# Optimization experiments

Measured on AMD Instinct MI355X. Metric: run time of the kernel, lower is better.

## Reference

```python
import jax, jax.numpy as jnp
import numpy as np

D_MODEL = 1024
D_COND = 512
N_HEADS = 16
D_HEAD = D_MODEL // N_HEADS
DIM_FF = 4 * D_MODEL
EPS = 1e-5


def setup_inputs() -> dict:
    key = jax.random.key(0)
    ks = jax.random.split(key, 12)
    B, S = 2, 2048
    s = 0.02
    return {
        "x": jax.random.normal(ks[0], (B, S, D_MODEL), jnp.float32),
        "cond": jax.random.normal(ks[1], (B, S, D_COND), jnp.float32),
        # AdaLN1 proj (stored as (in, out) so y = h @ W + b)
        "p1_w": jax.random.normal(ks[2], (D_COND, 2 * D_MODEL), jnp.float32) * s,
        "p1_b": jax.random.normal(ks[3], (2 * D_MODEL,), jnp.float32) * s,
        "qkv_w": jax.random.normal(ks[4], (D_MODEL, 3 * D_MODEL), jnp.float32) * s,
        "attn_out_w": jax.random.normal(ks[5], (D_MODEL, D_MODEL), jnp.float32) * s,
        "p2_w": jax.random.normal(ks[6], (D_COND, 2 * D_MODEL), jnp.float32) * s,
        "p2_b": jax.random.normal(ks[7], (2 * D_MODEL,), jnp.float32) * s,
        "ffn_w1": jax.random.normal(ks[8], (D_MODEL, DIM_FF), jnp.float32) * s,
        "ffn_b1": jax.random.normal(ks[9], (DIM_FF,), jnp.float32) * s,
        "ffn_w2": jax.random.normal(ks[10], (DIM_FF, D_MODEL), jnp.float32) * s,
        "ffn_b2": jax.random.normal(ks[11], (D_MODEL,), jnp.float32) * s,
    }


def _adaln(x, cond, w, b):
    # LayerNorm without affine, then (1+gamma)*xn + beta with gamma,beta from cond
    gb = jax.nn.silu(cond) @ w + b            # (B,S,2D)
    gamma, beta = jnp.split(gb, 2, axis=-1)
    mu = jnp.mean(x, axis=-1, keepdims=True)
    var = jnp.mean((x - mu) ** 2, axis=-1, keepdims=True)
    xn = (x - mu) * jax.lax.rsqrt(var + EPS)
    return xn * (1.0 + gamma) + beta


def reference(x, cond, p1_w, p1_b, qkv_w, attn_out_w, p2_w, p2_b,
              ffn_w1, ffn_b1, ffn_w2, ffn_b2):
    B, S, D = x.shape
    H, d = N_HEADS, D_HEAD
    scale = d ** -0.5

    residual = x
    h = _adaln(x, cond, p1_w, p1_b)
    qkv = h @ qkv_w                            # (B,S,3D)
    q, k, v = jnp.split(qkv, 3, axis=-1)
    q = q.reshape(B, S, H, d).transpose(0, 2, 1, 3)   # (B,H,S,d)
    k = k.reshape(B, S, H, d).transpose(0, 2, 1, 3)
    v = v.reshape(B, S, H, d).transpose(0, 2, 1, 3)

    scores = jnp.einsum("bhqd,bhkd->bhqk", q, k) * scale
    attn = jax.nn.softmax(scores, axis=-1)
    out = jnp.einsum("bhqk,bhkd->bhqd", attn, v)      # (B,H,S,d)
    out = out.transpose(0, 2, 1, 3).reshape(B, S, D)
    x = residual + out @ attn_out_w

    residual = x
    h = _adaln(x, cond, p2_w, p2_b)
    ff = jax.nn.gelu(h @ ffn_w1 + ffn_b1, approximate=False) @ ffn_w2 + ffn_b2
    return residual + ff
```

## Files before the change

### kernel.cpp

```cpp
#include <hip/hip_runtime.h>
#include <math.h>

#define D_MODEL 1024
#define SEQ 2048
#define NTOK 4096

typedef __attribute__((ext_vector_type(8))) short bf16x8;
typedef __attribute__((ext_vector_type(4))) float f32x4;

__device__ __forceinline__ unsigned short f2bf(float f) {
    union { float f; unsigned u; } v; v.f = f;
    unsigned r = v.u + 0x7FFFu + ((v.u >> 16) & 1u);
    return (unsigned short)(r >> 16);
}
__device__ __forceinline__ float bf2f(unsigned short u) {
    union { unsigned u; float f; } v; v.u = ((unsigned)u) << 16; return v.f;
}
__device__ __forceinline__ unsigned cvt_pk_bf16(float x, float y) {
    unsigned r;
    asm("v_cvt_pk_bf16_f32 %0, %1, %2" : "=v"(r) : "v"(x), "v"(y));
    return r;
}

__device__ __forceinline__ void ld_g2l(const void* g, void* l) {
    __builtin_amdgcn_global_load_lds(
        (const __attribute__((address_space(1))) void*)g,
        (__attribute__((address_space(3))) void*)l, 16, 0, 0);
}

__global__ __launch_bounds__(256) void prep_weights(
    const float* __restrict__ p1, const float* __restrict__ p2,
    const float* __restrict__ qkvw, const float* __restrict__ attnw,
    const float* __restrict__ f1, const float* __restrict__ f2,
    const float* __restrict__ cond,
    unsigned short* __restrict__ wt_cond, unsigned short* __restrict__ wt_qkv,
    unsigned short* __restrict__ wt_attn, unsigned short* __restrict__ wt_ffn1,
    unsigned short* __restrict__ wt_ffn2, unsigned short* __restrict__ siluc)
{
    const int t = blockIdx.x;
    if (t >= 3584) {
        const int base = (t - 3584) * 1024 + threadIdx.x;
#pragma unroll
        for (int i = 0; i < 4; i++) {
            const int idx = base + i * 256;
            float4 v = ((const float4*)cond)[idx];
            ushort4 o;
            o.x = f2bf(v.x / (1.f + expf(-v.x)));
            o.y = f2bf(v.y / (1.f + expf(-v.y)));
            o.z = f2bf(v.z / (1.f + expf(-v.z)));
            o.w = f2bf(v.w / (1.f + expf(-v.w)));
            ((ushort4*)siluc)[idx] = o;
        }
        return;
    }
    const float* src; unsigned short* dst; int K, N, lt;
    if (t < 512)       { src = (t < 256) ? p1 : p2;
                         dst = wt_cond + (t < 256 ? 0 : 2048 * 512);
                         K = 512;  N = 2048; lt = t & 255; }
    else if (t < 1280) { src = qkvw;  dst = wt_qkv;  K = 1024; N = 3072; lt = t - 512; }
    else if (t < 1536) { src = attnw; dst = wt_attn; K = 1024; N = 1024; lt = t - 1280; }
    else if (t < 2560) { src = f1;    dst = wt_ffn1; K = 1024; N = 4096; lt = t - 1536; }
    else               { src = f2;    dst = wt_ffn2; K = 4096; N = 1024; lt = t - 2560; }
    const int ntile = N >> 6;
    const int n0 = (lt % ntile) * 64, k0 = (lt / ntile) * 64;

    __shared__ float tile[64][65];
    const int tx = threadIdx.x & 15, ty = threadIdx.x >> 4;
#pragma unroll
    for (int i = 0; i < 4; i++) {
        const int k = ty + i * 16;
        float4 v = *(const float4*)&src[(size_t)(k0 + k) * N + n0 + tx * 4];
        tile[k][tx * 4 + 0] = v.x; tile[k][tx * 4 + 1] = v.y;
        tile[k][tx * 4 + 2] = v.z; tile[k][tx * 4 + 3] = v.w;
    }
    __syncthreads();
#pragma unroll
    for (int i = 0; i < 4; i++) {
        const int n = ty + i * 16;
        ushort4 o;
        o.x = f2bf(tile[tx * 4 + 0][n]); o.y = f2bf(tile[tx * 4 + 1][n]);
        o.z = f2bf(tile[tx * 4 + 2][n]); o.w = f2bf(tile[tx * 4 + 3][n]);
        *(ushort4*)&dst[(size_t)(n0 + n) * K + k0 + tx * 4] = o;
    }
}

#define EPI_GB   0
#define EPI_QKV  1
#define EPI_PROJ 2
#define EPI_FFN1 3
#define EPI_FFN2 4
#define EPI_PART 5

template<int EPI, int BM, int SPLIT = 1>
__global__ __launch_bounds__(256, 4) void gemm_bf16(
    const unsigned short* __restrict__ A,
    const unsigned short* __restrict__ Bt,
    const float* __restrict__ bias, const float* __restrict__ bias2,
    const float* __restrict__ res,
    void* __restrict__ Cv,
    unsigned short* __restrict__ qb, unsigned short* __restrict__ kb,
    unsigned short* __restrict__ vtb,
    int K)
{
    constexpr int WM = BM / 2;
    constexpr int MT = WM / 16;
    __shared__ __align__(16) unsigned short As[BM * 64];
    __shared__ __align__(16) unsigned short Bs[128 * 64];
    const int tid = threadIdx.x;
    const int lane = tid & 63, w = tid >> 6;
    const int cc = lane & 15, quad = lane >> 4;
    const int wm = (w >> 1) * WM, wn = (w & 1) * 64;
    const int m0 = blockIdx.y * BM, n0 = blockIdx.x * 128;
    const int kslice = K / SPLIT;
    const int kbeg = (SPLIT > 1) ? (int)blockIdx.z * kslice : 0;

    f32x4 acc[MT][4];
#pragma unroll
    for (int i = 0; i < MT; i++)
#pragma unroll
        for (int j = 0; j < 4; j++) acc[i][j] = (f32x4)0.f;

    for (int k0 = kbeg; k0 < kbeg + kslice; k0 += 64) {
        __syncthreads();
#pragma unroll
        for (int i = 0; i < BM / 32; i++) {
            const int idx = i * 256 + tid;
            const int row = idx >> 3, c = idx & 7;
            const int kc = (c ^ (row & 7)) << 3;
            ld_g2l(&A[(size_t)(m0 + row) * K + k0 + kc], &As[idx << 3]);
        }
#pragma unroll
        for (int i = 0; i < 4; i++) {
            const int idx = i * 256 + tid;
            const int row = idx >> 3, c = idx & 7;
            const int kc = (c ^ (row & 7)) << 3;
            ld_g2l(&Bt[(size_t)(n0 + row) * K + k0 + kc], &Bs[idx << 3]);
        }
        __syncthreads();
#pragma unroll
        for (int ks = 0; ks < 2; ks++) {
            bf16x8 af[MT], bfr[4];
            const int pc = (((ks << 2) | quad) ^ (cc & 7)) << 3;
#pragma unroll
            for (int t = 0; t < MT; t++)
                af[t]  = *(const bf16x8*)&As[(wm + t * 16 + cc) * 64 + pc];
#pragma unroll
            for (int t = 0; t < 4; t++)
                bfr[t] = *(const bf16x8*)&Bs[(wn + t * 16 + cc) * 64 + pc];
#pragma unroll
            for (int mt = 0; mt < MT; mt++)
#pragma unroll
                for (int nt = 0; nt < 4; nt++)
                    acc[mt][nt] = __builtin_amdgcn_mfma_f32_16x16x32_bf16(
                        af[mt], bfr[nt], acc[mt][nt], 0, 0, 0);
        }
    }

    if (EPI == EPI_GB) {
        unsigned short* C = (unsigned short*)Cv;
#pragma unroll
        for (int mt = 0; mt < MT; mt++)
#pragma unroll
        for (int r = 0; r < 4; r++) {
            const int m = m0 + wm + mt * 16 + quad * 4 + r;
#pragma unroll
            for (int nt = 0; nt < 4; nt++) {
                const int n = n0 + wn + nt * 16 + cc;
                const float b = (n < 2048) ? bias[n] : bias2[n - 2048];
                C[(size_t)m * 4096 + n] = f2bf(acc[mt][nt][r] + b);
            }
        }
    } else if (EPI == EPI_PROJ) {
        float* C = (float*)Cv;
#pragma unroll
        for (int mt = 0; mt < MT; mt++)
#pragma unroll
        for (int r = 0; r < 4; r++) {
            const int m = m0 + wm + mt * 16 + quad * 4 + r;
#pragma unroll
            for (int nt = 0; nt < 4; nt++) {
                const int n = n0 + wn + nt * 16 + cc;
                C[(size_t)m * 1024 + n] = acc[mt][nt][r] + res[(size_t)m * 1024 + n];
            }
        }
    } else if (EPI == EPI_FFN1) {
        unsigned short* C = (unsigned short*)Cv;
#pragma unroll
        for (int mt = 0; mt < MT; mt++)
#pragma unroll
        for (int r = 0; r < 4; r++) {
            const int m = m0 + wm + mt * 16 + quad * 4 + r;
#pragma unroll
            for (int nt = 0; nt < 4; nt++) {
                const int n = n0 + wn + nt * 16 + cc;
                float v = acc[mt][nt][r] + bias[n];
                const float u = v + 0.044715f * v * v * v;
                const float g = v / (1.f + exp2f(-2.3022084f * u));
                C[(size_t)m * 4096 + n] = f2bf(g);
            }
        }
    } else if (EPI == EPI_PART) {
        unsigned short* C = (unsigned short*)Cv + (size_t)blockIdx.z * (4096ull * 1024ull);
#pragma unroll
        for (int mt = 0; mt < MT; mt++)
#pragma unroll
        for (int r = 0; r < 4; r++) {
            const int m = m0 + wm + mt * 16 + quad * 4 + r;
#pragma unroll
            for (int nt = 0; nt < 4; nt++) {
                const int n = n0 + wn + nt * 16 + cc;
                C[(size_t)m * 1024 + n] = f2bf(acc[mt][nt][r]);
            }
        }
    } else if (EPI == EPI_FFN2) {
        float* C = (float*)Cv;
#pragma unroll
        for (int mt = 0; mt < MT; mt++)
#pragma unroll
        for (int r = 0; r < 4; r++) {
            const int m = m0 + wm + mt * 16 + quad * 4 + r;
#pragma unroll
            for (int nt = 0; nt < 4; nt++) {
                const int n = n0 + wn + nt * 16 + cc;
                C[(size_t)m * 1024 + n] = acc[mt][nt][r] + bias[n] + res[(size_t)m * 1024 + n];
            }
        }
    } else {
        const int region = n0 >> 10;
        const int b = m0 >> 11;
        if (region < 2) {
            unsigned short* dst = region ? kb : qb;
            const float sc = region ? 1.0f : 0.125f * 1.44269504088896340736f;
#pragma unroll
            for (int mt = 0; mt < MT; mt++)
#pragma unroll
            for (int r = 0; r < 4; r++) {
                const int m = m0 + wm + mt * 16 + quad * 4 + r;
                const int s = m & 2047;
#pragma unroll
                for (int nt = 0; nt < 4; nt++) {
                    const int n = (n0 + wn + nt * 16 + cc) & 1023;
                    const int hh = n >> 6, d = n & 63;
                    dst[(((size_t)b * 16 + hh) * 2048 + s) * 64 + d] =
                        f2bf(acc[mt][nt][r] * sc);
                }
            }
        } else {
            const int sb = (m0 + wm) & 2047;
#pragma unroll
            for (int mt = 0; mt < MT; mt++) {
                const int kpos = sb + ((mt >> 1) << 5) + (quad << 3) + ((mt & 1) << 2);
#pragma unroll
                for (int nt = 0; nt < 4; nt++) {
                    const int n = (n0 + wn + nt * 16 + cc) & 1023;
                    const int hh = n >> 6, d = n & 63;
                    ushort4 o;
                    o.x = f2bf(acc[mt][nt][0]); o.y = f2bf(acc[mt][nt][1]);
                    o.z = f2bf(acc[mt][nt][2]); o.w = f2bf(acc[mt][nt][3]);
                    *(ushort4*)&vtb[(((size_t)b * 16 + hh) * 64 + d) * 2048 + kpos] = o;
                }
            }
        }
    }
}

__global__ __launch_bounds__(256) void merge_ffn2(
    const unsigned short* __restrict__ P, const float* __restrict__ x1,
    const float* __restrict__ b2, float* __restrict__ out)
{
    const size_t idx = (size_t)blockIdx.x * 1024 + (size_t)threadIdx.x * 4;
    const int n = (int)(idx & 1023);
    float4 xv = *(const float4*)&x1[idx];
    float4 bv = *(const float4*)&b2[n];
    float s0 = 0.f, s1 = 0.f, s2 = 0.f, s3 = 0.f;
#pragma unroll
    for (int z = 0; z < 4; z++) {
        ushort4 p = *(const ushort4*)&P[z * (4096ull * 1024ull) + idx];
        s0 += bf2f(p.x); s1 += bf2f(p.y); s2 += bf2f(p.z); s3 += bf2f(p.w);
    }
    float4 o;
    o.x = xv.x + bv.x + s0;
    o.y = xv.y + bv.y + s1;
    o.z = xv.z + bv.z + s2;
    o.w = xv.w + bv.w + s3;
    *(float4*)&out[idx] = o;
}

__global__ __launch_bounds__(512) void attn_mfma(
    const unsigned short* __restrict__ qb, const unsigned short* __restrict__ kb,
    const unsigned short* __restrict__ vtb,
    unsigned short* __restrict__ Op0, unsigned short* __restrict__ Op1,
    unsigned short* __restrict__ Op2, unsigned short* __restrict__ Op3,
    float* __restrict__ lp)
{
    __shared__ __align__(16) unsigned short ks[64 * 64];
    __shared__ __align__(16) unsigned short vts[64 * 64];

    const int tid = threadIdx.x;
    const int lane = tid & 63, w = tid >> 6;
    const int c = lane & 15, quad = lane >> 4;
    const int bh = blockIdx.y;
    const int q0 = blockIdx.x * 256;
    const int z = blockIdx.z;
    const int kk0 = z * 512;

    bf16x8 qf[2][2];
#pragma unroll
    for (int qs = 0; qs < 2; qs++) {
        const size_t base = (((size_t)bh * 2048) + q0 + w * 32 + qs * 16 + c) * 64 + quad * 8;
        qf[qs][0] = *(const bf16x8*)&qb[base];
        qf[qs][1] = *(const bf16x8*)&qb[base + 32];
    }

    bf16x8 ones;
#pragma unroll
    for (int i = 0; i < 8; i++) ones[i] = (short)0x3F80;

    f32x4 of[2][4];
#pragma unroll
    for (int qs = 0; qs < 2; qs++)
#pragma unroll
        for (int i = 0; i < 4; i++) of[qs][i] = (f32x4)0.f;
    f32x4 lf[2];
    lf[0] = (f32x4)0.f; lf[1] = (f32x4)0.f;

    const size_t kbase = ((size_t)bh * 2048) * 64;
    const size_t vbase = ((size_t)bh * 64) * 2048;

    const int srow = tid >> 3, spc = tid & 7;
    const int slc = spc ^ (srow & 7);

    for (int kk = kk0; kk < kk0 + 512; kk += 64) {
        __syncthreads();
        ld_g2l(&kb[kbase + (size_t)(kk + srow) * 64 + slc * 8], &ks[tid << 3]);
        ld_g2l(&vtb[vbase + (size_t)srow * 2048 + kk + slc * 8], &vts[tid << 3]);
        __syncthreads();

        f32x4 sc[2][4];
#pragma unroll
        for (int qs = 0; qs < 2; qs++)
#pragma unroll
            for (int t = 0; t < 4; t++) sc[qs][t] = (f32x4)0.f;
#pragma unroll
        for (int t = 0; t < 4; t++) {
#pragma unroll
            for (int kh = 0; kh < 2; kh++) {
                const int phys = ((kh * 4 + quad) ^ (c & 7)) << 3;
                bf16x8 kf = *(const bf16x8*)&ks[(t * 16 + c) * 64 + phys];
#pragma unroll
                for (int qs = 0; qs < 2; qs++)
                    sc[qs][t] = __builtin_amdgcn_mfma_f32_16x16x32_bf16(
                        kf, qf[qs][kh], sc[qs][t], 0, 0, 0);
            }
        }

        bf16x8 pb[2][2];
#pragma unroll
        for (int qs = 0; qs < 2; qs++) {
#pragma unroll
            for (int t = 0; t < 4; t++)
#pragma unroll
                for (int r = 0; r < 4; r++)
                    sc[qs][t][r] = exp2f(sc[qs][t][r]);
#pragma unroll
            for (int kh = 0; kh < 2; kh++) {
                union { int4 i; bf16x8 v; } u;
                u.i.x = cvt_pk_bf16(sc[qs][2 * kh][0],     sc[qs][2 * kh][1]);
                u.i.y = cvt_pk_bf16(sc[qs][2 * kh][2],     sc[qs][2 * kh][3]);
                u.i.z = cvt_pk_bf16(sc[qs][2 * kh + 1][0], sc[qs][2 * kh + 1][1]);
                u.i.w = cvt_pk_bf16(sc[qs][2 * kh + 1][2], sc[qs][2 * kh + 1][3]);
                pb[qs][kh] = u.v;
            }
        }

#pragma unroll
        for (int qs = 0; qs < 2; qs++)
#pragma unroll
            for (int kh = 0; kh < 2; kh++)
                lf[qs] = __builtin_amdgcn_mfma_f32_16x16x32_bf16(
                    ones, pb[qs][kh], lf[qs], 0, 0, 0);

#pragma unroll
        for (int dt = 0; dt < 4; dt++) {
#pragma unroll
            for (int kh = 0; kh < 2; kh++) {
                const int phys = ((kh * 4 + quad) ^ (c & 7)) << 3;
                bf16x8 vf = *(const bf16x8*)&vts[(dt * 16 + c) * 64 + phys];
#pragma unroll
                for (int qs = 0; qs < 2; qs++)
                    of[qs][dt] = __builtin_amdgcn_mfma_f32_16x16x32_bf16(
                        vf, pb[qs][kh], of[qs][dt], 0, 0, 0);
            }
        }
    }

    unsigned short* Op = (z == 0) ? Op0 : (z == 1) ? Op1 : (z == 2) ? Op2 : Op3;
    const int b = bh >> 4, hh = bh & 15;
#pragma unroll
    for (int qs = 0; qs < 2; qs++) {
        const int q = q0 + w * 32 + qs * 16 + c;
        if (lane < 16)
            lp[((size_t)z * 32 + bh) * 2048 + q] = lf[qs][0];
        const size_t row = (size_t)(b * 2048 + q);
#pragma unroll
        for (int dt = 0; dt < 4; dt++) {
            ushort4 o;
            o.x = f2bf(of[qs][dt][0]); o.y = f2bf(of[qs][dt][1]);
            o.z = f2bf(of[qs][dt][2]); o.w = f2bf(of[qs][dt][3]);
            *(ushort4*)&Op[row * 1024 + hh * 64 + dt * 16 + quad * 4] = o;
        }
    }
}

__global__ __launch_bounds__(256) void merge_attn(
    const unsigned short* __restrict__ Op0, const unsigned short* __restrict__ Op1,
    const unsigned short* __restrict__ Op2, const unsigned short* __restrict__ Op3,
    const float* __restrict__ lp, unsigned short* __restrict__ attnb)
{
    const int row = blockIdx.x;
    const int b = row >> 11, s = row & 2047;
    const int tid = threadIdx.x;
    const int n = tid * 4, h = tid >> 4;
    float lsum = 0.f;
#pragma unroll
    for (int z = 0; z < 4; z++)
        lsum += lp[((size_t)z * 32 + b * 16 + h) * 2048 + s];
    const float inv = 1.f / lsum;
    const size_t off = (size_t)row * 1024 + n;
    ushort4 a0 = *(const ushort4*)&Op0[off];
    ushort4 a1 = *(const ushort4*)&Op1[off];
    ushort4 a2 = *(const ushort4*)&Op2[off];
    ushort4 a3 = *(const ushort4*)&Op3[off];
    ushort4 o;
    o.x = f2bf((bf2f(a0.x) + bf2f(a1.x) + bf2f(a2.x) + bf2f(a3.x)) * inv);
    o.y = f2bf((bf2f(a0.y) + bf2f(a1.y) + bf2f(a2.y) + bf2f(a3.y)) * inv);
    o.z = f2bf((bf2f(a0.z) + bf2f(a1.z) + bf2f(a2.z) + bf2f(a3.z)) * inv);
    o.w = f2bf((bf2f(a0.w) + bf2f(a1.w) + bf2f(a2.w) + bf2f(a3.w)) * inv);
    *(ushort4*)&attnb[off] = o;
}

__global__ __launch_bounds__(256) void adaln_bf(
    const float* __restrict__ x, const unsigned short* __restrict__ gb, int gboff,
    unsigned short* __restrict__ h)
{
    const int row = blockIdx.x;
    const float* xr = x + (size_t)row * D_MODEL;
    float4 v = ((const float4*)xr)[threadIdx.x];
    float s = v.x + v.y + v.z + v.w;
    float ss = v.x * v.x + v.y * v.y + v.z * v.z + v.w * v.w;
#pragma unroll
    for (int off = 1; off < 64; off <<= 1) {
        s  += __shfl_xor(s, off, 64);
        ss += __shfl_xor(ss, off, 64);
    }
    __shared__ float red[8];
    const int wave = threadIdx.x >> 6;
    if ((threadIdx.x & 63) == 0) { red[wave] = s; red[4 + wave] = ss; }
    __syncthreads();
    s  = red[0] + red[1] + red[2] + red[3];
    ss = red[4] + red[5] + red[6] + red[7];
    const float mu = s * (1.f / 1024.f);
    const float var = ss * (1.f / 1024.f) - mu * mu;
    const float rstd = rsqrtf(var + 1e-5f);
    const int c = threadIdx.x * 4;
    ushort4 g4 = *(const ushort4*)&gb[(size_t)row * 4096 + gboff + c];
    ushort4 b4 = *(const ushort4*)&gb[(size_t)row * 4096 + gboff + 1024 + c];
    ushort4 o;
    o.x = f2bf((v.x - mu) * rstd * (1.f + bf2f(g4.x)) + bf2f(b4.x));
    o.y = f2bf((v.y - mu) * rstd * (1.f + bf2f(g4.y)) + bf2f(b4.y));
    o.z = f2bf((v.z - mu) * rstd * (1.f + bf2f(g4.z)) + bf2f(b4.z));
    o.w = f2bf((v.w - mu) * rstd * (1.f + bf2f(g4.w)) + bf2f(b4.w));
    *(ushort4*)&h[(size_t)row * 1024 + c] = o;
}

extern "C" void kernel_launch(void* const* d_in, const int* in_sizes, int n_in,
                              void* d_out, int out_size, void* d_ws, size_t ws_size,
                              hipStream_t stream)
{
    const float* x      = (const float*)d_in[0];
    const float* cond   = (const float*)d_in[1];
    const float* p1_w   = (const float*)d_in[2];
    const float* p1_b   = (const float*)d_in[3];
    const float* qkv_w  = (const float*)d_in[4];
    const float* attn_w = (const float*)d_in[5];
    const float* p2_w   = (const float*)d_in[6];
    const float* p2_b   = (const float*)d_in[7];
    const float* ffn_w1 = (const float*)d_in[8];
    const float* ffn_b1 = (const float*)d_in[9];
    const float* ffn_w2 = (const float*)d_in[10];
    const float* ffn_b2 = (const float*)d_in[11];
    float* out = (float*)d_out;

    char* ws = (char*)d_ws;
    const size_t MB = 1024ull * 1024ull;
    unsigned short* wt_cond = (unsigned short*)(ws);
    unsigned short* wt_qkv  = (unsigned short*)(ws + 4 * MB);
    unsigned short* wt_attn = (unsigned short*)(ws + 10 * MB);
    unsigned short* wt_ffn1 = (unsigned short*)(ws + 12 * MB);
    unsigned short* wt_ffn2 = (unsigned short*)(ws + 20 * MB);
    unsigned short* siluc   = (unsigned short*)(ws + 28 * MB);
    unsigned short* gb      = (unsigned short*)(ws + 32 * MB);
    unsigned short* h       = (unsigned short*)(ws + 64 * MB);
    float*          x1      = (float*)(ws + 72 * MB);
    unsigned short* qb      = (unsigned short*)(ws + 88 * MB);
    unsigned short* kb      = (unsigned short*)(ws + 96 * MB);
    unsigned short* vtb     = (unsigned short*)(ws + 104 * MB);
    unsigned short* attnb   = (unsigned short*)(ws + 112 * MB);
    unsigned short* ff1     = (unsigned short*)(ws + 88 * MB);
    unsigned short* Op0     = (unsigned short*)(ws);
    unsigned short* Op1     = (unsigned short*)(ws + 64 * MB);
    unsigned short* Op2     = (unsigned short*)(ws + 72 * MB);
    unsigned short* Op3     = (unsigned short*)(ws + 80 * MB);
    float*          lp      = (float*)(ws + 28 * MB);
    unsigned short* Pff     = (unsigned short*)(ws + 32 * MB);

    dim3 blk(256);

    prep_weights<<<dim3(4096), blk, 0, stream>>>(
        p1_w, p2_w, qkv_w, attn_w, ffn_w1, ffn_w2, cond,
        wt_cond, wt_qkv, wt_attn, wt_ffn1, wt_ffn2, siluc);

    gemm_bf16<EPI_GB, 128><<<dim3(32, 32), blk, 0, stream>>>(
        siluc, wt_cond, p1_b, p2_b, nullptr, gb, nullptr, nullptr, nullptr, 512);
    adaln_bf<<<NTOK, blk, 0, stream>>>(x, gb, 0, h);
    gemm_bf16<EPI_QKV, 128><<<dim3(24, 32), blk, 0, stream>>>(
        h, wt_qkv, nullptr, nullptr, nullptr, nullptr, qb, kb, vtb, 1024);
    attn_mfma<<<dim3(SEQ / 256, 32, 4), dim3(512), 0, stream>>>(
        qb, kb, vtb, Op0, Op1, Op2, Op3, lp);
    merge_attn<<<dim3(NTOK), blk, 0, stream>>>(Op0, Op1, Op2, Op3, lp, attnb);
    gemm_bf16<EPI_PROJ, 64><<<dim3(8, 64), blk, 0, stream>>>(
        attnb, wt_attn, nullptr, nullptr, x, x1, nullptr, nullptr, nullptr, 1024);
    adaln_bf<<<NTOK, blk, 0, stream>>>(x1, gb, 2048, h);
    gemm_bf16<EPI_FFN1, 128><<<dim3(32, 32), blk, 0, stream>>>(
        h, wt_ffn1, ffn_b1, nullptr, nullptr, ff1, nullptr, nullptr, nullptr, 1024);
    gemm_bf16<EPI_PART, 64, 4><<<dim3(8, 64, 4), blk, 0, stream>>>(
        ff1, wt_ffn2, nullptr, nullptr, nullptr, Pff, nullptr, nullptr, nullptr, 4096);
    merge_ffn2<<<dim3(4096), blk, 0, stream>>>(Pff, x1, ffn_b2, out);
}
```

Measured before the change: 399.4 us.

## Double-buffer LDS in GEMMs, reduce FFN2 split-K, and prioritize MFMA in attention

Adds an optional double-buffered LDS path to the bf16 GEMM so the next K-tile's loads are issued while the current tile is computed, with one barrier per iteration. This path is enabled for the attention output projection and FFN2. FFN2 now uses BM=128 and split-K 2 instead of BM=64 and split-K 4, and the merge kernel reads two partial buffers instead of four. The attention kernel drops the explicit zeroing of score accumulators by feeding a zero operand directly, and raises wave priority around its MFMA sections. Double buffering doubles LDS use per block, which may reduce occupancy. With a single barrier, the async global-to-LDS loads may also need extra waitcnt handling to stay correct.

```diff
diff --git a/kernel.cpp b/kernel.cpp
--- a/kernel.cpp
+++ b/kernel.cpp
@@ -91,7 +91,7 @@
 #define EPI_FFN2 4
 #define EPI_PART 5
 
-template<int EPI, int BM, int SPLIT = 1>
+template<int EPI, int BM, bool DBUF = false, int SPLIT = 1>
 __global__ __launch_bounds__(256, 4) void gemm_bf16(
     const unsigned short* __restrict__ A,
     const unsigned short* __restrict__ Bt,
@@ -104,8 +104,9 @@
 {
     constexpr int WM = BM / 2;
     constexpr int MT = WM / 16;
-    __shared__ __align__(16) unsigned short As[BM * 64];
-    __shared__ __align__(16) unsigned short Bs[128 * 64];
+    constexpr int NB = DBUF ? 2 : 1;
+    __shared__ __align__(16) unsigned short As[NB][BM * 64];
+    __shared__ __align__(16) unsigned short Bs[NB][128 * 64];
     const int tid = threadIdx.x;
     const int lane = tid & 63, w = tid >> 6;
     const int cc = lane & 15, quad = lane >> 4;
@@ -120,39 +121,57 @@
 #pragma unroll
         for (int j = 0; j < 4; j++) acc[i][j] = (f32x4)0.f;
 
-    for (int k0 = kbeg; k0 < kbeg + kslice; k0 += 64) {
-        __syncthreads();
+    auto stage = [&](int buf, int k0) {
 #pragma unroll
         for (int i = 0; i < BM / 32; i++) {
             const int idx = i * 256 + tid;
             const int row = idx >> 3, c = idx & 7;
             const int kc = (c ^ (row & 7)) << 3;
-            ld_g2l(&A[(size_t)(m0 + row) * K + k0 + kc], &As[idx << 3]);
+            ld_g2l(&A[(size_t)(m0 + row) * K + k0 + kc], &As[buf][idx << 3]);
         }
 #pragma unroll
         for (int i = 0; i < 4; i++) {
             const int idx = i * 256 + tid;
             const int row = idx >> 3, c = idx & 7;
             const int kc = (c ^ (row & 7)) << 3;
-            ld_g2l(&Bt[(size_t)(n0 + row) * K + k0 + kc], &Bs[idx << 3]);
-        }
-        __syncthreads();
+            ld_g2l(&Bt[(size_t)(n0 + row) * K + k0 + kc], &Bs[buf][idx << 3]);
+        }
+    };
+    auto compute = [&](int buf) {
 #pragma unroll
         for (int ks = 0; ks < 2; ks++) {
             bf16x8 af[MT], bfr[4];
             const int pc = (((ks << 2) | quad) ^ (cc & 7)) << 3;
 #pragma unroll
             for (int t = 0; t < MT; t++)
-                af[t]  = *(const bf16x8*)&As[(wm + t * 16 + cc) * 64 + pc];
+                af[t]  = *(const bf16x8*)&As[buf][(wm + t * 16 + cc) * 64 + pc];
 #pragma unroll
             for (int t = 0; t < 4; t++)
-                bfr[t] = *(const bf16x8*)&Bs[(wn + t * 16 + cc) * 64 + pc];
+                bfr[t] = *(const bf16x8*)&Bs[buf][(wn + t * 16 + cc) * 64 + pc];
 #pragma unroll
             for (int mt = 0; mt < MT; mt++)
 #pragma unroll
                 for (int nt = 0; nt < 4; nt++)
                     acc[mt][nt] = __builtin_amdgcn_mfma_f32_16x16x32_bf16(
                         af[mt], bfr[nt], acc[mt][nt], 0, 0, 0);
+        }
+    };
+
+    if (DBUF) {
+        stage(0, kbeg);
+        int cur = 0;
+        for (int k0 = kbeg; k0 < kbeg + kslice; k0 += 64) {
+            __syncthreads();
+            if (k0 + 64 < kbeg + kslice) stage(cur ^ 1, k0 + 64);
+            compute(cur);
+            cur ^= 1;
+        }
+    } else {
+        for (int k0 = kbeg; k0 < kbeg + kslice; k0 += 64) {
+            __syncthreads();
+            stage(0, k0);
+            __syncthreads();
+            compute(0);
         }
     }
 
@@ -272,17 +291,13 @@
     const int n = (int)(idx & 1023);
     float4 xv = *(const float4*)&x1[idx];
     float4 bv = *(const float4*)&b2[n];
-    float s0 = 0.f, s1 = 0.f, s2 = 0.f, s3 = 0.f;
-#pragma unroll
-    for (int z = 0; z < 4; z++) {
-        ushort4 p = *(const ushort4*)&P[z * (4096ull * 1024ull) + idx];
-        s0 += bf2f(p.x); s1 += bf2f(p.y); s2 += bf2f(p.z); s3 += bf2f(p.w);
-    }
+    ushort4 p0 = *(const ushort4*)&P[idx];
+    ushort4 p1 = *(const ushort4*)&P[(4096ull * 1024ull) + idx];
     float4 o;
-    o.x = xv.x + bv.x + s0;
-    o.y = xv.y + bv.y + s1;
-    o.z = xv.z + bv.z + s2;
-    o.w = xv.w + bv.w + s3;
+    o.x = xv.x + bv.x + bf2f(p0.x) + bf2f(p1.x);
+    o.y = xv.y + bv.y + bf2f(p0.y) + bf2f(p1.y);
+    o.z = xv.z + bv.z + bf2f(p0.z) + bf2f(p1.z);
+    o.w = xv.w + bv.w + bf2f(p0.w) + bf2f(p1.w);
     *(float4*)&out[idx] = o;
 }
 
@@ -315,6 +330,7 @@
     bf16x8 ones;
 #pragma unroll
     for (int i = 0; i < 8; i++) ones[i] = (short)0x3F80;
+    const f32x4 fz = (f32x4)0.f;
 
     f32x4 of[2][4];
 #pragma unroll
@@ -337,22 +353,19 @@
         __syncthreads();
 
         f32x4 sc[2][4];
-#pragma unroll
-        for (int qs = 0; qs < 2; qs++)
-#pragma unroll
-            for (int t = 0; t < 4; t++) sc[qs][t] = (f32x4)0.f;
+        __builtin_amdgcn_s_setprio(1);
 #pragma unroll
         for (int t = 0; t < 4; t++) {
-#pragma unroll
-            for (int kh = 0; kh < 2; kh++) {
-                const int phys = ((kh * 4 + quad) ^ (c & 7)) << 3;
-                bf16x8 kf = *(const bf16x8*)&ks[(t * 16 + c) * 64 + phys];
-#pragma unroll
-                for (int qs = 0; qs < 2; qs++)
-                    sc[qs][t] = __builtin_amdgcn_mfma_f32_16x16x32_bf16(
-                        kf, qf[qs][kh], sc[qs][t], 0, 0, 0);
-            }
-        }
+            const int phys0 = ((0 * 4 + quad) ^ (c & 7)) << 3;
+            const int phys1 = ((1 * 4 + quad) ^ (c & 7)) << 3;
+            bf16x8 kf0 = *(const bf16x8*)&ks[(t * 16 + c) * 64 + phys0];
+            sc[0][t] = __builtin_amdgcn_mfma_f32_16x16x32_bf16(kf0, qf[0][0], fz, 0, 0, 0);
+            sc[1][t] = __builtin_amdgcn_mfma_f32_16x16x32_bf16(kf0, qf[1][0], fz, 0, 0, 0);
+            bf16x8 kf1 = *(const bf16x8*)&ks[(t * 16 + c) * 64 + phys1];
+            sc[0][t] = __builtin_amdgcn_mfma_f32_16x16x32_bf16(kf1, qf[0][1], sc[0][t], 0, 0, 0);
+            sc[1][t] = __builtin_amdgcn_mfma_f32_16x16x32_bf16(kf1, qf[1][1], sc[1][t], 0, 0, 0);
+        }
+        __builtin_amdgcn_s_setprio(0);
 
         bf16x8 pb[2][2];
 #pragma unroll
@@ -373,6 +386,7 @@
             }
         }
 
+        __builtin_amdgcn_s_setprio(1);
 #pragma unroll
         for (int qs = 0; qs < 2; qs++)
 #pragma unroll
@@ -392,6 +406,7 @@
                         vf, pb[qs][kh], of[qs][dt], 0, 0, 0);
             }
         }
+        __builtin_amdgcn_s_setprio(0);
     }
 
     unsigned short* Op = (z == 0) ? Op0 : (z == 1) ? Op1 : (z == 2) ? Op2 : Op3;
@@ -528,12 +543,12 @@
     attn_mfma<<<dim3(SEQ / 256, 32, 4), dim3(512), 0, stream>>>(
         qb, kb, vtb, Op0, Op1, Op2, Op3, lp);
     merge_attn<<<dim3(NTOK), blk, 0, stream>>>(Op0, Op1, Op2, Op3, lp, attnb);
-    gemm_bf16<EPI_PROJ, 64><<<dim3(8, 64), blk, 0, stream>>>(
+    gemm_bf16<EPI_PROJ, 64, true><<<dim3(8, 64), blk, 0, stream>>>(
         attnb, wt_attn, nullptr, nullptr, x, x1, nullptr, nullptr, nullptr, 1024);
     adaln_bf<<<NTOK, blk, 0, stream>>>(x1, gb, 2048, h);
     gemm_bf16<EPI_FFN1, 128><<<dim3(32, 32), blk, 0, stream>>>(
         h, wt_ffn1, ffn_b1, nullptr, nullptr, ff1, nullptr, nullptr, nullptr, 1024);
-    gemm_bf16<EPI_PART, 64, 4><<<dim3(8, 64, 4), blk, 0, stream>>>(
+    gemm_bf16<EPI_PART, 128, true, 2><<<dim3(8, 32, 2), blk, 0, stream>>>(
         ff1, wt_ffn2, nullptr, nullptr, nullptr, Pff, nullptr, nullptr, nullptr, 4096);
     merge_ffn2<<<dim3(4096), blk, 0, stream>>>(Pff, x1, ffn_b2, out);
 }
```

Measured after the change: 382.9 us. -4.1%, faster.
